# Performance work log

Measured on AMD Instinct MI355X. Metric: run time of the kernel, lower is better.

The kernel has to match this reference:

```python
import jax, jax.numpy as jnp
import numpy as np

IMG = 512
C = 3
PS = 16
G = 32
B = 64
NH = IMG // PS
NW = IMG // PS
NP_ = NH * NW
P2 = PS * PS


def setup_inputs() -> dict:
    key = jax.random.key(0)
    k1, k2, k3, k4 = jax.random.split(key, 4)
    x = jax.random.normal(k1, (B, C, IMG, IMG), dtype=jnp.float32)
    # Conv2d(1, ps*ps, kernel=ps) default init ~ U(-1/ps, 1/ps); scale random normals similarly.
    obfuscation_weights = jax.random.normal(k2, (C, G, P2, P2), dtype=jnp.float32) / PS
    obfuscation_biases = jax.random.normal(k3, (C, G, P2), dtype=jnp.float32) / PS
    channel_permutation = jax.random.permutation(k4, jnp.arange(C, dtype=jnp.int32))
    return {
        "x": x,
        "obfuscation_weights": obfuscation_weights,
        "obfuscation_biases": obfuscation_biases,
        "channel_permutation": channel_permutation,
    }


def reference(x, obfuscation_weights, obfuscation_biases, channel_permutation):
    # x: (B, C, H, W) -> patches (B, C, N, ps*ps)
    x_patched = (
        x.reshape(B, C, NH, PS, NW, PS)
        .transpose(0, 1, 2, 4, 3, 5)
        .reshape(B, C, NP_, P2)
    )
    # group index per spatial patch: (row + col) % group_size
    ridx = jnp.arange(NH)[:, None]
    cidx = jnp.arange(NW)[None, :]
    group_map = ((ridx + cidx) % G).reshape(-1)  # (N,)
    sel_w = obfuscation_weights[:, group_map]  # (C, N, P2, P2)
    sel_b = obfuscation_biases[:, group_map]  # (C, N, P2)
    out = jnp.einsum("bcnp,cnpo->bcno", x_patched, sel_w) + sel_b
    # back to image layout
    out = (
        out.reshape(B, C, NH, NW, PS, PS)
        .transpose(0, 1, 2, 4, 3, 5)
        .reshape(B, C, IMG, IMG)
    )
    out = out[:, channel_permutation]
    return jnp.tanh(out)
```

## Files before the change

### kernel.cpp

```cpp
#include <hip/hip_runtime.h>

#define C_SZ   3
#define IMG_SZ 512

typedef short  short8 __attribute__((ext_vector_type(8)));
typedef float  f32x4  __attribute__((ext_vector_type(4)));
typedef unsigned short u16;
typedef u16    u16x8  __attribute__((ext_vector_type(8)));

__device__ __forceinline__ u16 f2bf(float f) {
    unsigned u = __float_as_uint(f);
    u += 0x7FFFu + ((u >> 16) & 1u);
    return (u16)(u >> 16);
}

__device__ __forceinline__ float tanh_fast(float v) {
    float e = __expf(2.f * v);
    return 1.f - 2.f * __builtin_amdgcn_rcpf(e + 1.f);
}

__device__ __forceinline__ void gload_lds16(const float* g, float* l) {
    __builtin_amdgcn_global_load_lds(
        (const __attribute__((address_space(1))) void*)g,
        (__attribute__((address_space(3))) void*)l, 16, 0, 0);
}

__device__ __forceinline__ short8 gload_b128(const u16* p) {
    short8 d;
    asm volatile("global_load_dwordx4 %0, %1, off"
                 : "=v"(d) : "v"(p) : "memory");
    return d;
}

__global__ __launch_bounds__(256)
void prep_wt(const float* __restrict__ w, u16* __restrict__ wt) {
    const int cg = blockIdx.x;
    const int kb = blockIdx.y;
    __shared__ float T[32][260];
    const int tid = threadIdx.x;
    const float* wb = w + (size_t)cg * 65536 + (size_t)kb * 32 * 256;
    #pragma unroll
    for (int pass = 0; pass < 8; ++pass) {
        int q = pass * 256 + tid;
        int pl = q >> 6, o4 = (q & 63) * 4;
        float4 v = *reinterpret_cast<const float4*>(wb + (size_t)pl * 256 + o4);
        T[pl][o4 + 0] = v.x; T[pl][o4 + 1] = v.y;
        T[pl][o4 + 2] = v.z; T[pl][o4 + 3] = v.w;
    }
    __syncthreads();
    u16* dst = wt + ((size_t)cg * 8 + kb) * 8192;
    #pragma unroll
    for (int h0 = 0; h0 < 4; ++h0) {
        int h = h0 * 256 + tid;
        int kg = h >> 8, n = h & 255;
        u16x8 v;
        #pragma unroll
        for (int e = 0; e < 8; ++e) v[e] = f2bf(T[kg * 8 + e][n]);
        *reinterpret_cast<u16x8*>(dst + (size_t)kg * 2048 + n * 8) = v;
    }
}

__global__ __launch_bounds__(512)
void obf_mfma(const float* __restrict__ x,
              const u16*  __restrict__ wt,
              const float* __restrict__ bias,
              const int*  __restrict__ perm,
              float* __restrict__ out)
{
    const int bid  = blockIdx.x;
    const int xcd  = bid & 7;
    const int i    = bid >> 3;
    const int g    = i & 31;
    const int s    = xcd * 6 + (i >> 5);
    const int c    = s >> 4;
    const int mtile = s & 15;
    const int cg   = c * 32 + g;

    const int tid  = threadIdx.x;
    const int lane = tid & 63, wv = tid >> 6;
    const int wr   = wv >> 2, wc = wv & 3;
    const int r = lane & 15, kg = lane >> 4;

    __shared__ float As[4][4096];

    int cp = 0;
    #pragma unroll
    for (int ii = 0; ii < C_SZ; ++ii) if (perm[ii] == c) cp = ii;

    const float* g_src[2];
    #pragma unroll
    for (int j = 0; j < 2; ++j) {
        int q    = wv * 128 + j * 64 + lane;
        int row  = q >> 3;
        int lpos = (q & 7) ^ (row & 7);
        int mg   = mtile * 128 + row;
        int b    = mg >> 5, nh = mg & 31, nw = (g - nh) & 31;
        g_src[j] = x + (((size_t)(b * C_SZ + c) * IMG_SZ + nh * 16 + (lpos >> 2)) * IMG_SZ
                        + nw * 16 + (lpos & 3) * 4);
    }
    const u16* bsrc = wt + (size_t)cg * 65536 + kg * 2048 + (size_t)(wc * 64 + r) * 8;

    const int p0 = (((2 * kg)     ^ (r & 7)) * 4);
    const int p1 = (((2 * kg + 1) ^ (r & 7)) * 4);
    const int rbase = (wr * 64 + r) * 32;

    f32x4 acc[4][4] = {};
    short8 bv[2][4];

#define STAGE_A(t) do {                                                \
        float* d_ = &As[(t) & 3][0] + wv * 512;                        \
        gload_lds16(g_src[0] + (size_t)(t) * 1024, d_);                \
        gload_lds16(g_src[1] + (size_t)(t) * 1024, d_ + 256);          \
    } while (0)

    STAGE_A(0);
    STAGE_A(1);
    #pragma unroll
    for (int ni = 0; ni < 4; ++ni)
        bv[0][ni] = gload_b128(bsrc + ni * 128);

    #pragma unroll
    for (int t = 0; t < 8; ++t) {
        if (t < 7) {
            #pragma unroll
            for (int ni = 0; ni < 4; ++ni)
                bv[(t + 1) & 1][ni] = gload_b128(bsrc + (t + 1) * 8192 + ni * 128);
        }
        if (t < 6) STAGE_A(t + 2);

        if (t == 0 || t == 6) {
            asm volatile("s_waitcnt vmcnt(6)" ::: "memory");
        } else if (t <= 5) {
            asm volatile("s_waitcnt vmcnt(8)" ::: "memory");
        } else {
            asm volatile("s_waitcnt vmcnt(0)" ::: "memory");
        }
        __builtin_amdgcn_sched_barrier(0);
        __builtin_amdgcn_s_barrier();

        const float* lb = &As[t & 3][0];
        #pragma unroll
        for (int mi = 0; mi < 4; ++mi) {
            f32x4 v0 = *reinterpret_cast<const f32x4*>(lb + (rbase + mi * 16 * 32) + p0);
            f32x4 v1 = *reinterpret_cast<const f32x4*>(lb + (rbase + mi * 16 * 32) + p1);
            short8 af;
            af[0] = (short)f2bf(v0[0]); af[1] = (short)f2bf(v0[1]);
            af[2] = (short)f2bf(v0[2]); af[3] = (short)f2bf(v0[3]);
            af[4] = (short)f2bf(v1[0]); af[5] = (short)f2bf(v1[1]);
            af[6] = (short)f2bf(v1[2]); af[7] = (short)f2bf(v1[3]);
            #pragma unroll
            for (int ni = 0; ni < 4; ++ni)
                acc[mi][ni] = __builtin_amdgcn_mfma_f32_16x16x32_bf16(
                    af, bv[t & 1][ni], acc[mi][ni], 0, 0, 0);
        }
    }
#undef STAGE_A

    const int cc = lane & 15;
    float bs[4];
    #pragma unroll
    for (int ni = 0; ni < 4; ++ni)
        bs[ni] = bias[(size_t)cg * 256 + wc * 64 + ni * 16 + cc];

    #pragma unroll
    for (int mi = 0; mi < 4; ++mi) {
        #pragma unroll
        for (int reg = 0; reg < 4; ++reg) {
            const int ml = mi * 16 + kg * 4 + reg;
            const int mg = mtile * 128 + wr * 64 + ml;
            const int b  = mg >> 5, nh = mg & 31, nw = (g - nh) & 31;
            float* orow = out + ((size_t)(b * C_SZ + cp) * IMG_SZ + nh * 16) * IMG_SZ
                              + nw * 16 + cc;
            #pragma unroll
            for (int ni = 0; ni < 4; ++ni) {
                const int rp = wc * 4 + ni;
                orow[(size_t)rp * IMG_SZ] = tanh_fast(acc[mi][ni][reg] + bs[ni]);
            }
        }
    }
}

extern "C" void kernel_launch(void* const* d_in, const int* in_sizes, int n_in,
                              void* d_out, int out_size, void* d_ws, size_t ws_size,
                              hipStream_t stream) {
    const float* x    = (const float*)d_in[0];
    const float* w    = (const float*)d_in[1];
    const float* bias = (const float*)d_in[2];
    const int*   perm = (const int*)d_in[3];
    float* out = (float*)d_out;
    u16*   wt  = (u16*)d_ws;

    dim3 pgrid(C_SZ * 32, 8, 1);
    prep_wt<<<pgrid, 256, 0, stream>>>(w, wt);

    obf_mfma<<<1536, 512, 0, stream>>>(x, wt, bias, perm, out);
}
```

Before: 127.6 us.

## Swap MFMA operands for vectorized float4 stores and shrink A prefetch to three stages

The MFMA operands are swapped so each lane holds four consecutive output columns for one row. The epilogue can then load bias and write output as float4 instead of scattered scalar stores. The A-tile LDS ring is also cut from four buffers to three, with prefetch distance reduced from two steps to one. This lowers LDS use and may raise occupancy, at the cost of less latency hiding for global loads.

```diff
diff --git a/kernel.cpp b/kernel.cpp
--- a/kernel.cpp
+++ b/kernel.cpp
@@ -81,7 +81,7 @@
     const int wr   = wv >> 2, wc = wv & 3;
     const int r = lane & 15, kg = lane >> 4;
 
-    __shared__ float As[4][4096];
+    __shared__ float As[3][4096];
 
     int cp = 0;
     #pragma unroll
@@ -108,13 +108,12 @@
     short8 bv[2][4];
 
 #define STAGE_A(t) do {                                                \
-        float* d_ = &As[(t) & 3][0] + wv * 512;                        \
+        float* d_ = &As[(t) % 3][0] + wv * 512;                        \
         gload_lds16(g_src[0] + (size_t)(t) * 1024, d_);                \
         gload_lds16(g_src[1] + (size_t)(t) * 1024, d_ + 256);          \
     } while (0)
 
     STAGE_A(0);
-    STAGE_A(1);
     #pragma unroll
     for (int ni = 0; ni < 4; ++ni)
         bv[0][ni] = gload_b128(bsrc + ni * 128);
@@ -122,23 +121,18 @@
     #pragma unroll
     for (int t = 0; t < 8; ++t) {
         if (t < 7) {
+            STAGE_A(t + 1);
             #pragma unroll
             for (int ni = 0; ni < 4; ++ni)
                 bv[(t + 1) & 1][ni] = gload_b128(bsrc + (t + 1) * 8192 + ni * 128);
-        }
-        if (t < 6) STAGE_A(t + 2);
-
-        if (t == 0 || t == 6) {
             asm volatile("s_waitcnt vmcnt(6)" ::: "memory");
-        } else if (t <= 5) {
-            asm volatile("s_waitcnt vmcnt(8)" ::: "memory");
         } else {
             asm volatile("s_waitcnt vmcnt(0)" ::: "memory");
         }
         __builtin_amdgcn_sched_barrier(0);
         __builtin_amdgcn_s_barrier();
 
-        const float* lb = &As[t & 3][0];
+        const float* lb = &As[t % 3][0];
         #pragma unroll
         for (int mi = 0; mi < 4; ++mi) {
             f32x4 v0 = *reinterpret_cast<const f32x4*>(lb + (rbase + mi * 16 * 32) + p0);
@@ -151,31 +145,32 @@
             #pragma unroll
             for (int ni = 0; ni < 4; ++ni)
                 acc[mi][ni] = __builtin_amdgcn_mfma_f32_16x16x32_bf16(
-                    af, bv[t & 1][ni], acc[mi][ni], 0, 0, 0);
+                    bv[t & 1][ni], af, acc[mi][ni], 0, 0, 0);
         }
     }
 #undef STAGE_A
 
-    const int cc = lane & 15;
-    float bs[4];
+    const float* bb = bias + (size_t)cg * 256 + wc * 64 + kg * 4;
+    float4 bsv[4];
     #pragma unroll
     for (int ni = 0; ni < 4; ++ni)
-        bs[ni] = bias[(size_t)cg * 256 + wc * 64 + ni * 16 + cc];
+        bsv[ni] = *reinterpret_cast<const float4*>(bb + ni * 16);
 
     #pragma unroll
     for (int mi = 0; mi < 4; ++mi) {
+        const int mg = mtile * 128 + wr * 64 + mi * 16 + r;
+        const int b  = mg >> 5, nh = mg & 31, nw = (g - nh) & 31;
+        float* pbase = out + ((size_t)(b * C_SZ + cp) * IMG_SZ + nh * 16) * IMG_SZ
+                           + nw * 16 + kg * 4;
         #pragma unroll
-        for (int reg = 0; reg < 4; ++reg) {
-            const int ml = mi * 16 + kg * 4 + reg;
-            const int mg = mtile * 128 + wr * 64 + ml;
-            const int b  = mg >> 5, nh = mg & 31, nw = (g - nh) & 31;
-            float* orow = out + ((size_t)(b * C_SZ + cp) * IMG_SZ + nh * 16) * IMG_SZ
-                              + nw * 16 + cc;
-            #pragma unroll
-            for (int ni = 0; ni < 4; ++ni) {
-                const int rp = wc * 4 + ni;
-                orow[(size_t)rp * IMG_SZ] = tanh_fast(acc[mi][ni][reg] + bs[ni]);
-            }
+        for (int ni = 0; ni < 4; ++ni) {
+            const int rp = wc * 4 + ni;
+            float4 v;
+            v.x = tanh_fast(acc[mi][ni][0] + bsv[ni].x);
+            v.y = tanh_fast(acc[mi][ni][1] + bsv[ni].y);
+            v.z = tanh_fast(acc[mi][ni][2] + bsv[ni].z);
+            v.w = tanh_fast(acc[mi][ni][3] + bsv[ni].w);
+            *reinterpret_cast<float4*>(pbase + (size_t)rp * IMG_SZ) = v;
         }
     }
 }
```

New measurement: 126.2 us. No clear change (-1.1%).
